# Kernel tuning notes

Hardware: AMD Instinct MI355X
Metric: run time of the kernel (lower is better)

The kernel has to match this reference:

```python
import jax, jax.numpy as jnp
import numpy as np

B_, C_, H_, W_ = 32, 1, 512, 512
SMOOTH = 1.0


def _neighbors(im):
    # im: (N, H, W) bool. Returns the 8 neighbors P2..P9 (Zhang-Suen ordering:
    # N, NE, E, SE, S, SW, W, NW), zero-padded at the border.
    p = jnp.pad(im, ((0, 0), (1, 1), (1, 1)))
    P2 = p[:, :-2, 1:-1]
    P3 = p[:, :-2, 2:]
    P4 = p[:, 1:-1, 2:]
    P5 = p[:, 2:, 2:]
    P6 = p[:, 2:, 1:-1]
    P7 = p[:, 2:, :-2]
    P8 = p[:, 1:-1, :-2]
    P9 = p[:, :-2, :-2]
    return P2, P3, P4, P5, P6, P7, P8, P9


def _subiter(im, first: bool):
    P2, P3, P4, P5, P6, P7, P8, P9 = _neighbors(im)
    nb = [P2, P3, P4, P5, P6, P7, P8, P9]
    Bcnt = sum(n.astype(jnp.int32) for n in nb)          # number of set neighbors
    seq = nb + [P2]
    A = sum(((~seq[i]) & seq[i + 1]).astype(jnp.int32) for i in range(8))  # 0->1 transitions
    if first:
        cond = (~(P2 & P4 & P6)) & (~(P4 & P6 & P8))
    else:
        cond = (~(P2 & P4 & P8)) & (~(P2 & P6 & P8))
    remove = im & (Bcnt >= 2) & (Bcnt <= 6) & (A == 1) & cond
    return im & (~remove)


def _skeletonize(im):
    # Zhang-Suen thinning (the 2D algorithm skimage.morphology.skeletonize uses),
    # iterated to convergence. im: (N, H, W) bool.
    def body(state):
        cur, _ = state
        nxt = _subiter(_subiter(cur, True), False)
        return nxt, jnp.any(nxt != cur)

    def cond_fn(state):
        return state[1]

    out, _ = jax.lax.while_loop(cond_fn, body, (im, jnp.array(True)))
    return out


def _dilate_cross(im):
    # skimage.morphology.dilation with default cross-shaped (connectivity-1) footprint.
    p = jnp.pad(im, ((0, 0), (1, 1), (1, 1)))
    return im | p[:, :-2, 1:-1] | p[:, 2:, 1:-1] | p[:, 1:-1, :-2] | p[:, 1:-1, 2:]


def _skeleton_tube(y):
    # y: (B, C, H, W) int. Returns float skeleton (dilated twice) same shape.
    Bn, C, H, W = y.shape
    mask = y.reshape(Bn * C, H, W) > 0
    skel = _skeletonize(mask)
    skel = _dilate_cross(_dilate_cross(skel))
    return skel.reshape(Bn, C, H, W).astype(jnp.float32)


def setup_inputs() -> dict:
    key = jax.random.key(0)
    k1, k2 = jax.random.split(key)
    x = jax.random.uniform(k1, (B_, C_, H_, W_), dtype=jnp.float32)  # probabilities (apply_nonlin=None)
    y = jax.random.randint(k2, (B_, C_, H_, W_), 0, 2, dtype=jnp.int32)  # binary GT mask
    return {"x": x, "y": y}


def reference(x, y):
    y_skel = _skeleton_tube(y)                     # (B, C, H, W) float, constant wrt x
    axes = (2, 3)
    intersection = (x * y_skel).sum(axis=axes)     # (B, C)
    gt_sum = y_skel.sum(axis=axes)                 # (B, C)
    recall = (intersection + SMOOTH) / (gt_sum + SMOOTH)
    return -recall.mean()
```

## Files before the change

### kernel.cpp

```cpp
#include <hip/hip_runtime.h>
#include <stdint.h>

typedef unsigned long long u64;
typedef unsigned int u32;

#define BATCH 32
#define H 512
#define W 512
#define WPR 8
#define WORDS_IMG (H * WPR)
#define NPIX (H * W)

#define NSTRIP 8
#define OWN 64
#define NBLK (BATCH * NSTRIP)

#define HALO0 48
#define RL0 160
#define PAIRS0 24
#define THR0 640

#define WP 9
#define ERL 68

__global__ __launch_bounds__(256) void pack_kernel(const int* __restrict__ y,
                                                   u64* __restrict__ words,
                                                   int* __restrict__ flags,
                                                   int* __restrict__ counter) {
    if (blockIdx.x == 0 && threadIdx.x == 0) { flags[0] = 0; counter[0] = 0; }
    int gtid = blockIdx.x * blockDim.x + threadIdx.x;
    int lane = gtid & 63;
    int wave = gtid >> 6;
    const int* yb = y + (size_t)wave * 16 * 64;
    u64* wb = words + (size_t)wave * 16;
    int v[16];
    #pragma unroll
    for (int i = 0; i < 16; ++i) v[i] = yb[i * 64 + lane];
    #pragma unroll
    for (int i = 0; i < 16; ++i) {
        u64 m = __ballot(v[i] != 0);
        if (lane == 0) wb[i] = m;
    }
}

__device__ __forceinline__ void fulladd(u64 a, u64 b, u64 c, u64& s, u64& cy) {
    u64 t = a ^ b;
    s = t ^ c;
    cy = (a & b) | (t & c);
}

template<bool FIRST>
__device__ __forceinline__ u64 subiter2(const u64* __restrict__ src,
                                        u64* __restrict__ dst,
                                        int rg, int wc) {
    const int r = 2 * rg;
    u64 C[4], L[4], R[4];
    #pragma unroll
    for (int i = 0; i < 4; ++i) {
        int rr = r - 1 + i;
        bool v = (rr >= 0) && (rr < RL0);
        const u64* row = src + rr * WP;
        C[i] = v ? row[wc] : 0ull;
        L[i] = (v && wc > 0) ? row[wc - 1] : 0ull;
        R[i] = (v && wc < 7) ? row[wc + 1] : 0ull;
    }
    u64 Wst[4], Est[4];
    #pragma unroll
    for (int i = 0; i < 4; ++i) {
        Wst[i] = (C[i] << 1) | (L[i] >> 63);
        Est[i] = (C[i] >> 1) | (R[i] << 63);
    }
    u64 diff = 0;
    #pragma unroll
    for (int k = 0; k < 2; ++k) {
        u64 P2 = C[k],     P9 = Wst[k],     P3 = Est[k];
        u64 cC = C[k + 1], P8 = Wst[k + 1], P4 = Est[k + 1];
        u64 P6 = C[k + 2], P7 = Wst[k + 2], P5 = Est[k + 2];

        u64 s1, c1, s2, c2, s3, c3, ts, tc, us, uc;
        fulladd(P2, P3, P4, s1, c1);
        fulladd(P5, P6, P7, s2, c2);
        s3 = P8 ^ P9; c3 = P8 & P9;
        fulladd(s1, s2, s3, ts, tc);
        fulladd(c1, c2, c3, us, uc);
        u64 vs = us ^ tc, vc = us & tc;
        u64 w4 = uc ^ vc, w8 = uc & vc;
        u64 condB = (vs | w4 | w8) & ~(w8 | (w4 & vs & ts));

        u64 seen, multi, t;
        t = ~P2 & P3; seen = t;  multi = 0;
        t = ~P3 & P4; multi |= seen & t; seen |= t;
        t = ~P4 & P5; multi |= seen & t; seen |= t;
        t = ~P5 & P6; multi |= seen & t; seen |= t;
        t = ~P6 & P7; multi |= seen & t; seen |= t;
        t = ~P7 & P8; multi |= seen & t; seen |= t;
        t = ~P8 & P9; multi |= seen & t; seen |= t;
        t = ~P9 & P2; multi |= seen & t; seen |= t;
        u64 ex1 = seen & ~multi;

        u64 cond = FIRST ? (~(P2 & P4 & P6) & ~(P4 & P6 & P8))
                         : (~(P2 & P4 & P8) & ~(P2 & P6 & P8));

        u64 rem = cC & condB & ex1 & cond;
        u64 nw = cC & ~rem;
        dst[(r + k) * WP + wc] = nw;
        diff |= nw ^ cC;
    }
    return diff;
}

__global__ __launch_bounds__(THR0)
void strip_iter(const u64* __restrict__ gsrc, u64* __restrict__ gdst,
                int* __restrict__ flags) {
    __shared__ u64 A[RL0 * WP];
    __shared__ u64 Bf[RL0 * WP];
    __shared__ int s_any[2];

    const int tid = threadIdx.x;
    const int blk = blockIdx.x;
    const int b = blk >> 3;
    const int s = blk & 7;
    const int row0 = s * OWN;
    const int lane = tid & 63;
    const u64* src = gsrc + (size_t)b * WORDS_IMG;
    u64* dst = gdst + (size_t)b * WORDS_IMG;

    #pragma unroll
    for (int i = 0; i < 2; ++i) {
        int t = tid + i * THR0;
        int lrow = t >> 3, c = t & 7;
        int grow = row0 - HALO0 + lrow;
        u64 v = 0;
        if (grow >= 0 && grow < H) v = src[grow * WPR + c];
        A[lrow * WP + c] = v;
    }
    if (tid < 2) s_any[tid] = 0;
    __syncthreads();

    const int rg = tid >> 3;
    const int wc = tid & 7;
    const int rgLo = HALO0 / 2;
    const int rgHi = rgLo + OWN / 2;
    u64 lastown = 0;
    for (int pr = 0; pr < PAIRS0; ++pr) {
        u64 d1 = subiter2<true>(A, Bf, rg, wc);
        __syncthreads();
        u64 d2 = subiter2<false>(Bf, A, rg, wc);
        u64 d = d1 | d2;
        lastown = (rg >= rgLo && rg < rgHi) ? d : 0;
        int p = pr & 1;
        u64 bal = __ballot(d != 0);
        if (lane == 0 && bal) atomicOr(&s_any[p], 1);
        __syncthreads();
        int any = s_any[p];
        if (tid == 0) s_any[p ^ 1] = 0;
        if (!any) break;
    }

    if (rg >= rgLo && rg < rgHi) {
        int r = 2 * rg;
        dst[(row0 + r - HALO0) * WPR + wc]     = A[r * WP + wc];
        dst[(row0 + r - HALO0 + 1) * WPR + wc] = A[(r + 1) * WP + wc];
    }
    u64 bal = __ballot(lastown != 0);
    if (lane == 0 && bal) atomicOr(&flags[0], 1);
}

template<bool FIRST>
__device__ __forceinline__ void compute_sub_full(const u64* img, int wc, int r0,
                                                 u64 nw[8], u64& diff) {
    u64 C[10], L[10], R[10];
    #pragma unroll
    for (int i = 0; i < 10; ++i) {
        int rr = r0 - 1 + i;
        bool valid = (rr >= 0) && (rr < H);
        C[i] = valid ? img[rr * WPR + wc] : 0ull;
        L[i] = (valid && wc > 0) ? img[rr * WPR + wc - 1] : 0ull;
        R[i] = (valid && wc < WPR - 1) ? img[rr * WPR + wc + 1] : 0ull;
    }
    #pragma unroll
    for (int k = 0; k < 8; ++k) {
        u64 P2 = C[k];
        u64 P9 = (C[k]   << 1) | (L[k]   >> 63);
        u64 P3 = (C[k]   >> 1) | (R[k]   << 63);
        u64 cC = C[k+1];
        u64 P8 = (C[k+1] << 1) | (L[k+1] >> 63);
        u64 P4 = (C[k+1] >> 1) | (R[k+1] << 63);
        u64 P6 = C[k+2];
        u64 P7 = (C[k+2] << 1) | (L[k+2] >> 63);
        u64 P5 = (C[k+2] >> 1) | (R[k+2] << 63);

        u64 s1, c1, s2, c2, s3, c3, ts, tc, us, uc;
        fulladd(P2, P3, P4, s1, c1);
        fulladd(P5, P6, P7, s2, c2);
        s3 = P8 ^ P9; c3 = P8 & P9;
        fulladd(s1, s2, s3, ts, tc);
        fulladd(c1, c2, c3, us, uc);
        u64 vs = us ^ tc, vc = us & tc;
        u64 w4 = uc ^ vc, w8 = uc & vc;
        u64 condB = (vs | w4 | w8) & ~(w8 | (w4 & vs & ts));

        u64 seen, multi, t;
        t = ~P2 & P3; seen = t;  multi = 0;
        t = ~P3 & P4; multi |= seen & t; seen |= t;
        t = ~P4 & P5; multi |= seen & t; seen |= t;
        t = ~P5 & P6; multi |= seen & t; seen |= t;
        t = ~P6 & P7; multi |= seen & t; seen |= t;
        t = ~P7 & P8; multi |= seen & t; seen |= t;
        t = ~P8 & P9; multi |= seen & t; seen |= t;
        t = ~P9 & P2; multi |= seen & t; seen |= t;
        u64 ex1 = seen & ~multi;

        u64 cond = FIRST ? (~(P2 & P4 & P6) & ~(P4 & P6 & P8))
                         : (~(P2 & P4 & P8) & ~(P2 & P6 & P8));

        u64 rem = cC & condB & ex1 & cond;
        nw[k] = cC & ~rem;
        diff |= nw[k] ^ cC;
    }
}

__global__ __launch_bounds__(512)
void fallback_kernel(u64* __restrict__ gimg0, const int* __restrict__ flags) {
    if (flags[0] == 0) return;

    __shared__ u64 img[WORDS_IMG];
    __shared__ int s_changed;
    const int b = blockIdx.x;
    const int tid = threadIdx.x;
    const int wc = tid & 7;
    const int r0 = (tid >> 3) * 8;
    u64* gimg = gimg0 + (size_t)b * WORDS_IMG;

    #pragma unroll
    for (int k = 0; k < 8; ++k)
        img[(r0 + k) * WPR + wc] = gimg[(r0 + k) * WPR + wc];
    if (tid == 0) s_changed = 0;
    __syncthreads();

    bool changed = true;
    for (int it = 0; it < 4096 && changed; ++it) {
        u64 diff = 0;
        u64 nw[8];
        compute_sub_full<true>(img, wc, r0, nw, diff);
        __syncthreads();
        #pragma unroll
        for (int k = 0; k < 8; ++k) img[(r0 + k) * WPR + wc] = nw[k];
        __syncthreads();
        compute_sub_full<false>(img, wc, r0, nw, diff);
        __syncthreads();
        #pragma unroll
        for (int k = 0; k < 8; ++k) img[(r0 + k) * WPR + wc] = nw[k];
        if (diff) atomicOr(&s_changed, 1);
        __syncthreads();
        changed = (s_changed != 0);
        __syncthreads();
        if (tid == 0) s_changed = 0;
    }

    #pragma unroll
    for (int k = 0; k < 8; ++k)
        gimg[(r0 + k) * WPR + wc] = img[(r0 + k) * WPR + wc];
}

__global__ __launch_bounds__(512)
void tail_kernel(const u64* __restrict__ gB, const float* __restrict__ x,
                 float* __restrict__ partial, int* __restrict__ partial_gt,
                 int* __restrict__ counter, float* __restrict__ out) {
    __shared__ u64 D[ERL * WP];
    __shared__ u64 E[ERL * WP];
    __shared__ float s_red[8];
    __shared__ int s_pc[8];
    __shared__ int s_last;

    const int tid = threadIdx.x;
    const int blk = blockIdx.x;
    const int b = blk >> 3;
    const int s = blk & 7;
    const int row0 = s * OWN;
    const int lane = tid & 63;
    const int wv = tid >> 6;
    const u64* src = gB + (size_t)b * WORDS_IMG;

    for (int t = tid; t < ERL * 8; t += 512) {
        int lrow = t >> 3, c = t & 7;
        int grow = row0 - 2 + lrow;
        u64 v = 0;
        if (grow >= 0 && grow < H) v = src[grow * WPR + c];
        D[lrow * WP + c] = v;
    }
    __syncthreads();

    for (int t = tid; t < ERL * 8; t += 512) {
        int l = t >> 3, c = t & 7;
        int grow = row0 - 2 + l;
        u64 v = 0;
        if (grow >= 0 && grow < H) {
            u64 cc = D[l * WP + c];
            u64 up = (l > 0)       ? D[(l - 1) * WP + c] : 0ull;
            u64 dn = (l < ERL - 1) ? D[(l + 1) * WP + c] : 0ull;
            u64 lw = (c > 0) ? D[l * WP + c - 1] : 0ull;
            u64 rw = (c < 7) ? D[l * WP + c + 1] : 0ull;
            v = cc | up | dn | ((cc << 1) | (lw >> 63)) | ((cc >> 1) | (rw << 63));
        }
        E[l * WP + c] = v;
    }
    __syncthreads();

    const int l = 2 + (tid >> 3);
    const int c = tid & 7;
    u64 v;
    {
        u64 cc = E[l * WP + c];
        u64 up = E[(l - 1) * WP + c];
        u64 dn = E[(l + 1) * WP + c];
        u64 lw = (c > 0) ? E[l * WP + c - 1] : 0ull;
        u64 rw = (c < 7) ? E[l * WP + c + 1] : 0ull;
        v = cc | up | dn | ((cc << 1) | (lw >> 63)) | ((cc >> 1) | (rw << 63));
    }
    int pc = __popcll(v);
    for (int off = 32; off >= 1; off >>= 1) pc += __shfl_down(pc, off, 64);
    if (lane == 0) s_pc[wv] = pc;
    __syncthreads();
    D[l * WP + c] = v;
    __syncthreads();

    const float4* x4 = (const float4*)(x + (size_t)b * NPIX + (size_t)row0 * W);
    const int quad = tid & 127;
    const int rgp  = tid >> 7;
    const int wi   = quad >> 4;
    const int sh   = (quad & 15) * 4;
    float s0 = 0.0f, s1 = 0.0f, s2 = 0.0f, s3 = 0.0f;
    #pragma unroll 4
    for (int i = 0; i < 16; ++i) {
        int rrow = i * 4 + rgp;
        u64 word = D[(2 + rrow) * WP + wi];
        u32 bits = (u32)(word >> sh) & 0xFu;
        float4 v4 = x4[rrow * 128 + quad];
        s0 = fmaf((float)(bits & 1u),        v4.x, s0);
        s1 = fmaf((float)((bits >> 1) & 1u), v4.y, s1);
        s2 = fmaf((float)((bits >> 2) & 1u), v4.z, s2);
        s3 = fmaf((float)((bits >> 3) & 1u), v4.w, s3);
    }
    float sum = (s0 + s1) + (s2 + s3);
    for (int off = 32; off >= 1; off >>= 1) sum += __shfl_down(sum, off, 64);
    if (lane == 0) s_red[wv] = sum;
    __syncthreads();

    if (tid == 0) {
        float fs = 0.0f;
        int is = 0;
        #pragma unroll
        for (int k = 0; k < 8; ++k) { fs += s_red[k]; is += s_pc[k]; }
        __hip_atomic_store(&partial[blk], fs, __ATOMIC_RELAXED,
                           __HIP_MEMORY_SCOPE_AGENT);
        __hip_atomic_store(&partial_gt[blk], is, __ATOMIC_RELAXED,
                           __HIP_MEMORY_SCOPE_AGENT);
        int prev = __hip_atomic_fetch_add(counter, 1, __ATOMIC_ACQ_REL,
                                          __HIP_MEMORY_SCOPE_AGENT);
        s_last = (prev == NBLK - 1);
    }
    __syncthreads();

    if (s_last && tid < 32) {
        float inter = 0.0f;
        int g = 0;
        #pragma unroll
        for (int j = 0; j < 8; ++j) {
            inter += __hip_atomic_load(&partial[tid * 8 + j], __ATOMIC_RELAXED,
                                       __HIP_MEMORY_SCOPE_AGENT);
            g += __hip_atomic_load(&partial_gt[tid * 8 + j], __ATOMIC_RELAXED,
                                   __HIP_MEMORY_SCOPE_AGENT);
        }
        float rec = (inter + 1.0f) / ((float)g + 1.0f);
        #pragma unroll
        for (int off = 16; off >= 1; off >>= 1)
            rec += __shfl_down(rec, off, 32);
        if (tid == 0) out[0] = -(rec / 32.0f);
    }
}

extern "C" void kernel_launch(void* const* d_in, const int* in_sizes, int n_in,
                              void* d_out, int out_size, void* d_ws, size_t ws_size,
                              hipStream_t stream) {
    const float* x = (const float*)d_in[0];
    const int*   y = (const int*)d_in[1];
    float* out = (float*)d_out;

    char* ws = (char*)d_ws;
    u64* gA = (u64*)ws;
    u64* gB = (u64*)(ws + (size_t)BATCH * WORDS_IMG * 8);
    int* flags = (int*)(ws + 2 * (size_t)BATCH * WORDS_IMG * 8);
    int* counter = flags + 4;
    float* partial = (float*)(counter + 4);
    int* partial_gt = (int*)(partial + NBLK);

    pack_kernel<<<2048, 256, 0, stream>>>(y, gA, flags, counter);
    strip_iter<<<NBLK, THR0, 0, stream>>>(gA, gB, flags);
    fallback_kernel<<<BATCH, 512, 0, stream>>>(gB, flags);
    tail_kernel<<<NBLK, 512, 0, stream>>>(gB, x, partial, partial_gt,
                                          counter, out);
}
```

Measured before the change: 49.99 us.

## Add smaller-halo strip pass with shrinking active region and conditional rescue tier

Thinning now starts with a strip kernel that uses a 32-row halo and 16 iteration pairs instead of 48 and 24. Each pair also shrinks the set of rows it processes, since rows near the halo edge can no longer influence the owned rows, which skips work that cannot matter. If owned rows are still changing, a rescue kernel reruns the original 48-halo pass, and the full-image fallback becomes a third tier. The tail kernel reads from whichever buffer holds the final result. This adds a kernel launch that usually exits early, plus extra buffer ping-pong logic.

```diff
diff --git a/kernel.cpp b/kernel.cpp
--- a/kernel.cpp
+++ b/kernel.cpp
@@ -15,6 +15,11 @@
 #define OWN 64
 #define NBLK (BATCH * NSTRIP)
 
+#define HALO1 32
+#define RL1 128
+#define PAIRS1 16
+#define THR1 512
+
 #define HALO0 48
 #define RL0 160
 #define PAIRS0 24
@@ -27,7 +32,9 @@
                                                    u64* __restrict__ words,
                                                    int* __restrict__ flags,
                                                    int* __restrict__ counter) {
-    if (blockIdx.x == 0 && threadIdx.x == 0) { flags[0] = 0; counter[0] = 0; }
+    if (blockIdx.x == 0 && threadIdx.x == 0) {
+        flags[0] = 0; flags[1] = 0; counter[0] = 0;
+    }
     int gtid = blockIdx.x * blockDim.x + threadIdx.x;
     int lane = gtid & 63;
     int wave = gtid >> 6;
@@ -49,7 +56,7 @@
     cy = (a & b) | (t & c);
 }
 
-template<bool FIRST>
+template<bool FIRST, int RLp>
 __device__ __forceinline__ u64 subiter2(const u64* __restrict__ src,
                                         u64* __restrict__ dst,
                                         int rg, int wc) {
@@ -58,7 +65,7 @@
     #pragma unroll
     for (int i = 0; i < 4; ++i) {
         int rr = r - 1 + i;
-        bool v = (rr >= 0) && (rr < RL0);
+        bool v = (rr >= 0) && (rr < RLp);
         const u64* row = src + rr * WP;
         C[i] = v ? row[wc] : 0ull;
         L[i] = (v && wc > 0) ? row[wc - 1] : 0ull;
@@ -109,11 +116,11 @@
     return diff;
 }
 
-__global__ __launch_bounds__(THR0)
-void strip_iter(const u64* __restrict__ gsrc, u64* __restrict__ gdst,
-                int* __restrict__ flags) {
-    __shared__ u64 A[RL0 * WP];
-    __shared__ u64 Bf[RL0 * WP];
+__global__ __launch_bounds__(THR1)
+void strip16(const u64* __restrict__ gsrc, u64* __restrict__ gdst,
+             int* __restrict__ flags) {
+    __shared__ u64 A[RL1 * WP];
+    __shared__ u64 Bf[RL1 * WP];
     __shared__ int s_any[2];
 
     const int tid = threadIdx.x;
@@ -127,6 +134,67 @@
 
     #pragma unroll
     for (int i = 0; i < 2; ++i) {
+        int t = tid + i * THR1;
+        int lrow = t >> 3, c = t & 7;
+        int grow = row0 - HALO1 + lrow;
+        u64 v = 0;
+        if (grow >= 0 && grow < H) v = src[grow * WPR + c];
+        A[lrow * WP + c] = v;
+    }
+    if (tid < 2) s_any[tid] = 0;
+    __syncthreads();
+
+    const int rg = tid >> 3;
+    const int wc = tid & 7;
+    u64 lastown = 0;
+    for (int pr = 0; pr < PAIRS1; ++pr) {
+        const int lo = 2 * pr + 1;
+        const int hi = 126 - 2 * pr;
+        const bool active = (2 * rg + 1 >= lo) && (2 * rg <= hi);
+        u64 d1 = 0, d2 = 0;
+        if (active) d1 = subiter2<true, RL1>(A, Bf, rg, wc);
+        __syncthreads();
+        if (active) d2 = subiter2<false, RL1>(Bf, A, rg, wc);
+        u64 d = d1 | d2;
+        lastown = (rg >= 16 && rg < 48) ? d : 0;
+        int p = pr & 1;
+        u64 bal = __ballot(d != 0);
+        if (lane == 0 && bal) atomicOr(&s_any[p], 1);
+        __syncthreads();
+        int any = s_any[p];
+        if (tid == 0) s_any[p ^ 1] = 0;
+        if (!any) break;
+    }
+
+    if (rg >= 16 && rg < 48) {
+        int r = 2 * rg;
+        dst[(row0 + r - HALO1) * WPR + wc]     = A[r * WP + wc];
+        dst[(row0 + r - HALO1 + 1) * WPR + wc] = A[(r + 1) * WP + wc];
+    }
+    u64 bal = __ballot(lastown != 0);
+    if (lane == 0 && bal) atomicOr(&flags[0], 1);
+}
+
+__global__ __launch_bounds__(THR0)
+void rescue_kernel(const u64* __restrict__ gsrc, u64* __restrict__ gdst,
+                   int* __restrict__ flags) {
+    if (flags[0] == 0) return;
+
+    __shared__ u64 A[RL0 * WP];
+    __shared__ u64 Bf[RL0 * WP];
+    __shared__ int s_any[2];
+
+    const int tid = threadIdx.x;
+    const int blk = blockIdx.x;
+    const int b = blk >> 3;
+    const int s = blk & 7;
+    const int row0 = s * OWN;
+    const int lane = tid & 63;
+    const u64* src = gsrc + (size_t)b * WORDS_IMG;
+    u64* dst = gdst + (size_t)b * WORDS_IMG;
+
+    #pragma unroll
+    for (int i = 0; i < 2; ++i) {
         int t = tid + i * THR0;
         int lrow = t >> 3, c = t & 7;
         int grow = row0 - HALO0 + lrow;
@@ -143,9 +211,9 @@
     const int rgHi = rgLo + OWN / 2;
     u64 lastown = 0;
     for (int pr = 0; pr < PAIRS0; ++pr) {
-        u64 d1 = subiter2<true>(A, Bf, rg, wc);
-        __syncthreads();
-        u64 d2 = subiter2<false>(Bf, A, rg, wc);
+        u64 d1 = subiter2<true, RL0>(A, Bf, rg, wc);
+        __syncthreads();
+        u64 d2 = subiter2<false, RL0>(Bf, A, rg, wc);
         u64 d = d1 | d2;
         lastown = (rg >= rgLo && rg < rgHi) ? d : 0;
         int p = pr & 1;
@@ -163,7 +231,7 @@
         dst[(row0 + r - HALO0 + 1) * WPR + wc] = A[(r + 1) * WP + wc];
     }
     u64 bal = __ballot(lastown != 0);
-    if (lane == 0 && bal) atomicOr(&flags[0], 1);
+    if (lane == 0 && bal) atomicOr(&flags[1], 1);
 }
 
 template<bool FIRST>
@@ -222,7 +290,7 @@
 
 __global__ __launch_bounds__(512)
 void fallback_kernel(u64* __restrict__ gimg0, const int* __restrict__ flags) {
-    if (flags[0] == 0) return;
+    if (flags[1] == 0) return;
 
     __shared__ u64 img[WORDS_IMG];
     __shared__ int s_changed;
@@ -264,9 +332,12 @@
 }
 
 __global__ __launch_bounds__(512)
-void tail_kernel(const u64* __restrict__ gB, const float* __restrict__ x,
+void tail_kernel(const u64* __restrict__ gA, const u64* __restrict__ gB,
+                 const int* __restrict__ flags, const float* __restrict__ x,
                  float* __restrict__ partial, int* __restrict__ partial_gt,
                  int* __restrict__ counter, float* __restrict__ out) {
+    const u64* cur = flags[0] ? gA : gB;
+
     __shared__ u64 D[ERL * WP];
     __shared__ u64 E[ERL * WP];
     __shared__ float s_red[8];
@@ -280,7 +351,7 @@
     const int row0 = s * OWN;
     const int lane = tid & 63;
     const int wv = tid >> 6;
-    const u64* src = gB + (size_t)b * WORDS_IMG;
+    const u64* src = cur + (size_t)b * WORDS_IMG;
 
     for (int t = tid; t < ERL * 8; t += 512) {
         int lrow = t >> 3, c = t & 7;
@@ -396,8 +467,9 @@
     int* partial_gt = (int*)(partial + NBLK);
 
     pack_kernel<<<2048, 256, 0, stream>>>(y, gA, flags, counter);
-    strip_iter<<<NBLK, THR0, 0, stream>>>(gA, gB, flags);
-    fallback_kernel<<<BATCH, 512, 0, stream>>>(gB, flags);
-    tail_kernel<<<NBLK, 512, 0, stream>>>(gB, x, partial, partial_gt,
-                                          counter, out);
-}
+    strip16<<<NBLK, THR1, 0, stream>>>(gA, gB, flags);
+    rescue_kernel<<<NBLK, THR0, 0, stream>>>(gB, gA, flags);
+    fallback_kernel<<<BATCH, 512, 0, stream>>>(gA, flags);
+    tail_kernel<<<NBLK, 512, 0, stream>>>(gA, gB, flags, x, partial,
+                                          partial_gt, counter, out);
+}
```

Result: faster. 45.88 us (-8.2%).

## Split strip thinning into smaller strips with a shrinking active region

Applied to the files above, without the earlier changes.

The strip thinning kernel now uses 16 strips of 32 owned rows with a 32-row halo instead of 8 strips of 64 rows with a 48-row halo. That launches twice as many smaller blocks and cuts redundant halo computation. Each iteration also skips rows whose results can no longer influence the owned region, because the valid band shrinks by one row per subiteration. The iteration cap drops to 16 pairs, so more images may fall through to the full-image fallback kernel when thinning has not converged within the halo.

```diff
diff --git a/kernel.cpp b/kernel.cpp
--- a/kernel.cpp
+++ b/kernel.cpp
@@ -11,17 +11,20 @@
 #define WORDS_IMG (H * WPR)
 #define NPIX (H * W)
 
-#define NSTRIP 8
-#define OWN 64
-#define NBLK (BATCH * NSTRIP)
-
-#define HALO0 48
-#define RL0 160
-#define PAIRS0 24
-#define THR0 640
+#define NSTRIP 16
+#define OWN 32
+#define HALO 32
+#define RL 96
+#define PAIRS 16
+#define THRS 384
+#define NBLKS (BATCH * NSTRIP)
+
+#define NSTRIP_T 8
+#define OWN_T 64
+#define NBLK_T (BATCH * NSTRIP_T)
+#define ERL 68
 
 #define WP 9
-#define ERL 68
 
 __global__ __launch_bounds__(256) void pack_kernel(const int* __restrict__ y,
                                                    u64* __restrict__ words,
@@ -49,7 +52,7 @@
     cy = (a & b) | (t & c);
 }
 
-template<bool FIRST>
+template<bool FIRST, int RLp>
 __device__ __forceinline__ u64 subiter2(const u64* __restrict__ src,
                                         u64* __restrict__ dst,
                                         int rg, int wc) {
@@ -58,7 +61,7 @@
     #pragma unroll
     for (int i = 0; i < 4; ++i) {
         int rr = r - 1 + i;
-        bool v = (rr >= 0) && (rr < RL0);
+        bool v = (rr >= 0) && (rr < RLp);
         const u64* row = src + rr * WP;
         C[i] = v ? row[wc] : 0ull;
         L[i] = (v && wc > 0) ? row[wc - 1] : 0ull;
@@ -109,17 +112,17 @@
     return diff;
 }
 
-__global__ __launch_bounds__(THR0)
-void strip_iter(const u64* __restrict__ gsrc, u64* __restrict__ gdst,
-                int* __restrict__ flags) {
-    __shared__ u64 A[RL0 * WP];
-    __shared__ u64 Bf[RL0 * WP];
+__global__ __launch_bounds__(THRS)
+void strip_kernel(const u64* __restrict__ gsrc, u64* __restrict__ gdst,
+                  int* __restrict__ flags) {
+    __shared__ u64 A[RL * WP];
+    __shared__ u64 Bf[RL * WP];
     __shared__ int s_any[2];
 
     const int tid = threadIdx.x;
     const int blk = blockIdx.x;
-    const int b = blk >> 3;
-    const int s = blk & 7;
+    const int b = blk >> 4;
+    const int s = blk & 15;
     const int row0 = s * OWN;
     const int lane = tid & 63;
     const u64* src = gsrc + (size_t)b * WORDS_IMG;
@@ -127,9 +130,9 @@
 
     #pragma unroll
     for (int i = 0; i < 2; ++i) {
-        int t = tid + i * THR0;
+        int t = tid + i * THRS;
         int lrow = t >> 3, c = t & 7;
-        int grow = row0 - HALO0 + lrow;
+        int grow = row0 - HALO + lrow;
         u64 v = 0;
         if (grow >= 0 && grow < H) v = src[grow * WPR + c];
         A[lrow * WP + c] = v;
@@ -139,15 +142,17 @@
 
     const int rg = tid >> 3;
     const int wc = tid & 7;
-    const int rgLo = HALO0 / 2;
-    const int rgHi = rgLo + OWN / 2;
     u64 lastown = 0;
-    for (int pr = 0; pr < PAIRS0; ++pr) {
-        u64 d1 = subiter2<true>(A, Bf, rg, wc);
-        __syncthreads();
-        u64 d2 = subiter2<false>(Bf, A, rg, wc);
+    for (int pr = 0; pr < PAIRS; ++pr) {
+        const int lo = 2 * pr + 1;
+        const int hi = 94 - 2 * pr;
+        const bool active = (2 * rg + 1 >= lo) && (2 * rg <= hi);
+        u64 d1 = 0, d2 = 0;
+        if (active) d1 = subiter2<true, RL>(A, Bf, rg, wc);
+        __syncthreads();
+        if (active) d2 = subiter2<false, RL>(Bf, A, rg, wc);
         u64 d = d1 | d2;
-        lastown = (rg >= rgLo && rg < rgHi) ? d : 0;
+        lastown = (rg >= 16 && rg < 32) ? d : 0;
         int p = pr & 1;
         u64 bal = __ballot(d != 0);
         if (lane == 0 && bal) atomicOr(&s_any[p], 1);
@@ -157,10 +162,10 @@
         if (!any) break;
     }
 
-    if (rg >= rgLo && rg < rgHi) {
+    if (rg >= 16 && rg < 32) {
         int r = 2 * rg;
-        dst[(row0 + r - HALO0) * WPR + wc]     = A[r * WP + wc];
-        dst[(row0 + r - HALO0 + 1) * WPR + wc] = A[(r + 1) * WP + wc];
+        dst[(row0 + r - HALO) * WPR + wc]     = A[r * WP + wc];
+        dst[(row0 + r - HALO + 1) * WPR + wc] = A[(r + 1) * WP + wc];
     }
     u64 bal = __ballot(lastown != 0);
     if (lane == 0 && bal) atomicOr(&flags[0], 1);
@@ -221,7 +226,7 @@
 }
 
 __global__ __launch_bounds__(512)
-void fallback_kernel(u64* __restrict__ gimg0, const int* __restrict__ flags) {
+void fullfix_kernel(u64* __restrict__ gimg0, const int* __restrict__ flags) {
     if (flags[0] == 0) return;
 
     __shared__ u64 img[WORDS_IMG];
@@ -277,7 +282,7 @@
     const int blk = blockIdx.x;
     const int b = blk >> 3;
     const int s = blk & 7;
-    const int row0 = s * OWN;
+    const int row0 = s * OWN_T;
     const int lane = tid & 63;
     const int wv = tid >> 6;
     const u64* src = gB + (size_t)b * WORDS_IMG;
@@ -358,7 +363,7 @@
                            __HIP_MEMORY_SCOPE_AGENT);
         int prev = __hip_atomic_fetch_add(counter, 1, __ATOMIC_ACQ_REL,
                                           __HIP_MEMORY_SCOPE_AGENT);
-        s_last = (prev == NBLK - 1);
+        s_last = (prev == NBLK_T - 1);
     }
     __syncthreads();
 
@@ -393,11 +398,11 @@
     int* flags = (int*)(ws + 2 * (size_t)BATCH * WORDS_IMG * 8);
     int* counter = flags + 4;
     float* partial = (float*)(counter + 4);
-    int* partial_gt = (int*)(partial + NBLK);
+    int* partial_gt = (int*)(partial + NBLK_T);
 
     pack_kernel<<<2048, 256, 0, stream>>>(y, gA, flags, counter);
-    strip_iter<<<NBLK, THR0, 0, stream>>>(gA, gB, flags);
-    fallback_kernel<<<BATCH, 512, 0, stream>>>(gB, flags);
-    tail_kernel<<<NBLK, 512, 0, stream>>>(gB, x, partial, partial_gt,
-                                          counter, out);
-}
+    strip_kernel<<<NBLKS, THRS, 0, stream>>>(gA, gB, flags);
+    fullfix_kernel<<<BATCH, 512, 0, stream>>>(gB, flags);
+    tail_kernel<<<NBLK_T, 512, 0, stream>>>(gB, x, partial, partial_gt,
+                                            counter, out);
+}
```

Measured after the change: 50.32 us. No clear change (+0.6%).

## Shrink strip halo, skip converged-out rows, prefetch x in tail kernel

Applied to the files above, without the earlier changes.

The strip thinning kernel now uses a 32-row halo with at most 16 iteration pairs and 512 threads, instead of a 48-row halo with 24 pairs. Each pair only computes on a shrinking window of rows that can still affect the owned rows, so invalid halo work is skipped. The tail kernel loads all of its x values into registers before the bitmask and dilation work, so global loads overlap that compute. The smaller halo makes it more likely that the full-image fallback must run when convergence is slow, and the prefetch raises register use.

```diff
diff --git a/kernel.cpp b/kernel.cpp
--- a/kernel.cpp
+++ b/kernel.cpp
@@ -15,10 +15,10 @@
 #define OWN 64
 #define NBLK (BATCH * NSTRIP)
 
-#define HALO0 48
-#define RL0 160
-#define PAIRS0 24
-#define THR0 640
+#define HALO1 32
+#define RL1 128
+#define PAIRS1 16
+#define THR1 512
 
 #define WP 9
 #define ERL 68
@@ -49,7 +49,7 @@
     cy = (a & b) | (t & c);
 }
 
-template<bool FIRST>
+template<bool FIRST, int RLp>
 __device__ __forceinline__ u64 subiter2(const u64* __restrict__ src,
                                         u64* __restrict__ dst,
                                         int rg, int wc) {
@@ -58,7 +58,7 @@
     #pragma unroll
     for (int i = 0; i < 4; ++i) {
         int rr = r - 1 + i;
-        bool v = (rr >= 0) && (rr < RL0);
+        bool v = (rr >= 0) && (rr < RLp);
         const u64* row = src + rr * WP;
         C[i] = v ? row[wc] : 0ull;
         L[i] = (v && wc > 0) ? row[wc - 1] : 0ull;
@@ -109,11 +109,11 @@
     return diff;
 }
 
-__global__ __launch_bounds__(THR0)
-void strip_iter(const u64* __restrict__ gsrc, u64* __restrict__ gdst,
-                int* __restrict__ flags) {
-    __shared__ u64 A[RL0 * WP];
-    __shared__ u64 Bf[RL0 * WP];
+__global__ __launch_bounds__(THR1)
+void strip16(const u64* __restrict__ gsrc, u64* __restrict__ gdst,
+             int* __restrict__ flags) {
+    __shared__ u64 A[RL1 * WP];
+    __shared__ u64 Bf[RL1 * WP];
     __shared__ int s_any[2];
 
     const int tid = threadIdx.x;
@@ -127,9 +127,9 @@
 
     #pragma unroll
     for (int i = 0; i < 2; ++i) {
-        int t = tid + i * THR0;
+        int t = tid + i * THR1;
         int lrow = t >> 3, c = t & 7;
-        int grow = row0 - HALO0 + lrow;
+        int grow = row0 - HALO1 + lrow;
         u64 v = 0;
         if (grow >= 0 && grow < H) v = src[grow * WPR + c];
         A[lrow * WP + c] = v;
@@ -139,15 +139,17 @@
 
     const int rg = tid >> 3;
     const int wc = tid & 7;
-    const int rgLo = HALO0 / 2;
-    const int rgHi = rgLo + OWN / 2;
     u64 lastown = 0;
-    for (int pr = 0; pr < PAIRS0; ++pr) {
-        u64 d1 = subiter2<true>(A, Bf, rg, wc);
-        __syncthreads();
-        u64 d2 = subiter2<false>(Bf, A, rg, wc);
+    for (int pr = 0; pr < PAIRS1; ++pr) {
+        const int lo = 2 * pr + 1;
+        const int hi = 126 - 2 * pr;
+        const bool active = (2 * rg + 1 >= lo) && (2 * rg <= hi);
+        u64 d1 = 0, d2 = 0;
+        if (active) d1 = subiter2<true, RL1>(A, Bf, rg, wc);
+        __syncthreads();
+        if (active) d2 = subiter2<false, RL1>(Bf, A, rg, wc);
         u64 d = d1 | d2;
-        lastown = (rg >= rgLo && rg < rgHi) ? d : 0;
+        lastown = (rg >= 16 && rg < 48) ? d : 0;
         int p = pr & 1;
         u64 bal = __ballot(d != 0);
         if (lane == 0 && bal) atomicOr(&s_any[p], 1);
@@ -157,10 +159,10 @@
         if (!any) break;
     }
 
-    if (rg >= rgLo && rg < rgHi) {
+    if (rg >= 16 && rg < 48) {
         int r = 2 * rg;
-        dst[(row0 + r - HALO0) * WPR + wc]     = A[r * WP + wc];
-        dst[(row0 + r - HALO0 + 1) * WPR + wc] = A[(r + 1) * WP + wc];
+        dst[(row0 + r - HALO1) * WPR + wc]     = A[r * WP + wc];
+        dst[(row0 + r - HALO1 + 1) * WPR + wc] = A[(r + 1) * WP + wc];
     }
     u64 bal = __ballot(lastown != 0);
     if (lane == 0 && bal) atomicOr(&flags[0], 1);
@@ -221,7 +223,7 @@
 }
 
 __global__ __launch_bounds__(512)
-void fallback_kernel(u64* __restrict__ gimg0, const int* __restrict__ flags) {
+void fullfix_kernel(u64* __restrict__ gimg0, const int* __restrict__ flags) {
     if (flags[0] == 0) return;
 
     __shared__ u64 img[WORDS_IMG];
@@ -281,6 +283,14 @@
     const int lane = tid & 63;
     const int wv = tid >> 6;
     const u64* src = gB + (size_t)b * WORDS_IMG;
+
+    const float4* x4 = (const float4*)(x + (size_t)b * NPIX + (size_t)row0 * W);
+    const int quad = tid & 127;
+    const int rgp  = tid >> 7;
+    float4 xv[16];
+    #pragma unroll
+    for (int i = 0; i < 16; ++i)
+        xv[i] = x4[(i * 4 + rgp) * 128 + quad];
 
     for (int t = tid; t < ERL * 8; t += 512) {
         int lrow = t >> 3, c = t & 7;
@@ -325,22 +335,18 @@
     D[l * WP + c] = v;
     __syncthreads();
 
-    const float4* x4 = (const float4*)(x + (size_t)b * NPIX + (size_t)row0 * W);
-    const int quad = tid & 127;
-    const int rgp  = tid >> 7;
-    const int wi   = quad >> 4;
-    const int sh   = (quad & 15) * 4;
+    const int wi = quad >> 4;
+    const int sh = (quad & 15) * 4;
     float s0 = 0.0f, s1 = 0.0f, s2 = 0.0f, s3 = 0.0f;
-    #pragma unroll 4
+    #pragma unroll
     for (int i = 0; i < 16; ++i) {
         int rrow = i * 4 + rgp;
         u64 word = D[(2 + rrow) * WP + wi];
         u32 bits = (u32)(word >> sh) & 0xFu;
-        float4 v4 = x4[rrow * 128 + quad];
-        s0 = fmaf((float)(bits & 1u),        v4.x, s0);
-        s1 = fmaf((float)((bits >> 1) & 1u), v4.y, s1);
-        s2 = fmaf((float)((bits >> 2) & 1u), v4.z, s2);
-        s3 = fmaf((float)((bits >> 3) & 1u), v4.w, s3);
+        s0 = fmaf((float)(bits & 1u),        xv[i].x, s0);
+        s1 = fmaf((float)((bits >> 1) & 1u), xv[i].y, s1);
+        s2 = fmaf((float)((bits >> 2) & 1u), xv[i].z, s2);
+        s3 = fmaf((float)((bits >> 3) & 1u), xv[i].w, s3);
     }
     float sum = (s0 + s1) + (s2 + s3);
     for (int off = 32; off >= 1; off >>= 1) sum += __shfl_down(sum, off, 64);
@@ -396,8 +402,8 @@
     int* partial_gt = (int*)(partial + NBLK);
 
     pack_kernel<<<2048, 256, 0, stream>>>(y, gA, flags, counter);
-    strip_iter<<<NBLK, THR0, 0, stream>>>(gA, gB, flags);
-    fallback_kernel<<<BATCH, 512, 0, stream>>>(gB, flags);
+    strip16<<<NBLK, THR1, 0, stream>>>(gA, gB, flags);
+    fullfix_kernel<<<BATCH, 512, 0, stream>>>(gB, flags);
     tail_kernel<<<NBLK, 512, 0, stream>>>(gB, x, partial, partial_gt,
                                           counter, out);
 }
```

New measurement: 44.25 us. 11.5% less time.
